# Performance work log

Hardware: AMD Instinct MI355X
Metric: run time of the kernel (lower is better)

The kernel has to match this reference:

```python
import jax, jax.numpy as jnp
from jax import lax
import numpy as np

DN = ('NHWC', 'HWIO', 'NHWC')  # NHWC activations, HWIO kernels (TF layout)
EPS = 1e-3


def setup_inputs() -> dict:
    key = jax.random.key(0)
    ks = jax.random.split(key, 6)
    B, H, W, C = 16, 64, 64, 256
    x = jax.random.normal(ks[0], (B, H, W, C), jnp.float32)
    # per-sample predicted kernels (scaled to keep activations well-conditioned)
    depthwise_kernels = jax.random.normal(ks[1], (B, 3, 3, C, C), jnp.float32) * 0.02
    pointwise_kernels = jax.random.normal(ks[2], (B, 1, 1, C, C), jnp.float32) * 0.06
    biases = jax.random.normal(ks[3], (B, C), jnp.float32) * 0.1
    # shared trailing Conv2D layer params
    conv_w = jax.random.normal(ks[4], (3, 3, C, C), jnp.float32) * 0.02
    conv_b = jnp.zeros((C,), jnp.float32)
    return dict(x=x, depthwise_kernels=depthwise_kernels,
                pointwise_kernels=pointwise_kernels, biases=biases,
                conv_w=conv_w, conv_b=conv_b)


def _instance_norm(x):
    # tf.nn.moments over spatial dims (population variance), eps=0.001
    mean = jnp.mean(x, axis=(1, 2), keepdims=True)
    var = jnp.var(x, axis=(1, 2), keepdims=True)
    return (x - mean) * lax.rsqrt(var + EPS)


def _reflect_pad_hw(x, p=1):
    pad = [(0, 0)] * (x.ndim - 3) + [(p, p), (p, p), (0, 0)]
    return jnp.pad(x, pad, mode='reflect')


def _per_sample_conv(xi, dk, pk, bi):
    # xi: [H,W,C]; dk: [3,3,C,Cm]; pk: [1,1,Cm,Co]; bi: [Co]
    xp = _reflect_pad_hw(xi)[None]  # [1,H+2,W+2,C]
    y = lax.conv_general_dilated(xp, dk, (1, 1), 'VALID', dimension_numbers=DN)
    y = lax.conv_general_dilated(y, pk, (1, 1), 'VALID', dimension_numbers=DN)
    return (y + bi)[0]


def reference(x, depthwise_kernels, pointwise_kernels, biases, conv_w, conv_b):
    x = _instance_norm(x)
    # per-sample kernels -> vmap over batch (replaces tf.map_fn)
    x = jax.vmap(_per_sample_conv)(x, depthwise_kernels, pointwise_kernels, biases)
    # shared Conv2D: reflect pad + VALID conv + bias
    xp = _reflect_pad_hw(x)
    y = lax.conv_general_dilated(xp, conv_w, (1, 1), 'VALID', dimension_numbers=DN)
    return y + conv_b
```

## Files before the change

kernel.cpp:

```cpp
#include <hip/hip_runtime.h>


typedef __bf16 bf16x8 __attribute__((ext_vector_type(8)));
typedef float f32x4 __attribute__((ext_vector_type(4)));

__device__ __forceinline__ float bf2f(unsigned short v) {
    return __uint_as_float(((unsigned int)v) << 16);
}
__device__ __forceinline__ unsigned short f2bf(float f) {
    unsigned int u = __float_as_uint(f);
    unsigned int r = (u + 0x7FFFu + ((u >> 16) & 1u)) >> 16;
    return (unsigned short)r;
}
__device__ __forceinline__ float ldg_elem(const void* p, size_t idx, bool isbf) {
    return isbf ? bf2f(((const unsigned short*)p)[idx]) : ((const float*)p)[idx];
}

__device__ __forceinline__ void gload16(const void* g, void* l) {
    __builtin_amdgcn_global_load_lds(
        (__attribute__((address_space(1))) void*)(unsigned long long)g,
        (__attribute__((address_space(3))) void*)(unsigned long long)l,
        16, 0, 0);
}

#define RAW_BARRIER() do { asm volatile("" ::: "memory"); \
                           __builtin_amdgcn_s_barrier();   \
                           asm volatile("" ::: "memory"); } while (0)

template <bool DO_DK>
__global__ void prep_kernel(const void* __restrict__ x, const void* __restrict__ pk,
                            const void* __restrict__ cw, const void* __restrict__ dk,
                            float* __restrict__ partS, float* __restrict__ partQ,
                            unsigned short* __restrict__ pkT, unsigned short* __restrict__ cwT,
                            unsigned short* __restrict__ dkT, int* __restrict__ flagp) {
    __shared__ int wild;
    __shared__ float red[4][64][9];
    __shared__ unsigned short tile[64][66];
    const int t = threadIdx.x;
    if (t == 0) wild = 0;
    __syncthreads();
    int cnt = 0;
    for (int i = 0; i < 16; ++i) {
        float a = fabsf(bf2f(((const unsigned short*)x)[t * 16 + i]));
        if (!(a < 64.f) || (a != 0.f && a < 1e-5f)) cnt++;
    }
    atomicAdd(&wild, cnt);
    __syncthreads();
    const bool isbf = (wild <= 512);
    const int id = blockIdx.x;
    if (id == 0 && t == 0) *flagp = isbf ? 1 : 0;

    if (id < 512) {
        const int b = id >> 5, ch = id & 31;
        const int l = t & 63;
        const int c4 = l * 4;
        const int sp0 = t >> 6;
        const size_t base = ((size_t)(b * 4096 + ch * 128 + sp0)) * 256 + c4;
        float s[4] = {0.f, 0.f, 0.f, 0.f}, q[4] = {0.f, 0.f, 0.f, 0.f};
        if (isbf) {
            for (int i = 0; i < 32; ++i) {
                ushort4 v = *(const ushort4*)((const unsigned short*)x + base + (size_t)i * 1024);
                float a[4] = {bf2f(v.x), bf2f(v.y), bf2f(v.z), bf2f(v.w)};
#pragma unroll
                for (int j = 0; j < 4; ++j) { s[j] += a[j]; q[j] += a[j] * a[j]; }
            }
        } else {
            for (int i = 0; i < 32; ++i) {
                float4 v = *(const float4*)((const float*)x + base + (size_t)i * 1024);
                float a[4] = {v.x, v.y, v.z, v.w};
#pragma unroll
                for (int j = 0; j < 4; ++j) { s[j] += a[j]; q[j] += a[j] * a[j]; }
            }
        }
#pragma unroll
        for (int j = 0; j < 4; ++j) { red[sp0][l][j] = s[j]; red[sp0][l][4 + j] = q[j]; }
        __syncthreads();
        if (t < 64) {
#pragma unroll
            for (int j = 0; j < 4; ++j) {
                float ss = red[0][t][j] + red[1][t][j] + red[2][t][j] + red[3][t][j];
                float qq = red[0][t][4 + j] + red[1][t][4 + j] + red[2][t][4 + j] + red[3][t][4 + j];
                int c = t * 4 + j;
                partS[(b * 32 + ch) * 256 + c] = ss;
                partQ[(b * 32 + ch) * 256 + c] = qq;
            }
        }
        return;
    }

    const void* src; unsigned short* dst; int s_per; long bstride; int coStride; int q;
    if (id < 768)      { q = id - 512; src = pk; dst = pkT; s_per = 1; bstride = 65536L;  coStride = 256;  }
    else if (id < 912) { q = id - 768; src = cw; dst = cwT; s_per = 9; bstride = 0L;      coStride = 2304; }
    else               { if (!DO_DK) return;
                         q = id - 912; src = dk; dst = dkT; s_per = 9; bstride = 589824L; coStride = 2304; }
    const int sl = q >> 4;
    const int ci0 = ((q >> 2) & 3) * 64, co0 = (q & 3) * 64;
    const int b = sl / s_per;
    const size_t dbase = (size_t)b * (size_t)bstride + (size_t)(sl % s_per) * 256;
    const int co4 = (t & 15) * 4;
    const int r0 = t >> 4;
#pragma unroll
    for (int i = 0; i < 4; ++i) {
        int r = r0 + i * 16;
        size_t sidx = (size_t)sl * 65536 + (size_t)(ci0 + r) * 256 + co0 + co4;
        if (isbf) {
            ushort4 v = *(const ushort4*)((const unsigned short*)src + sidx);
            tile[r][co4] = v.x; tile[r][co4 + 1] = v.y;
            tile[r][co4 + 2] = v.z; tile[r][co4 + 3] = v.w;
        } else {
            float4 v = *(const float4*)((const float*)src + sidx);
            tile[r][co4] = f2bf(v.x); tile[r][co4 + 1] = f2bf(v.y);
            tile[r][co4 + 2] = f2bf(v.z); tile[r][co4 + 3] = f2bf(v.w);
        }
    }
    __syncthreads();
    const int cip = (t & 31) * 2;
    const int cob = t >> 5;
#pragma unroll
    for (int i = 0; i < 8; ++i) {
        int co = cob + i * 8;
        *(unsigned int*)(dst + dbase + (size_t)(co0 + co) * coStride + ci0 + cip) =
            (unsigned int)tile[cip][co] | ((unsigned int)tile[cip + 1][co] << 16);
    }
}

__global__ void norm_finalize2(const float* __restrict__ partS, const float* __restrict__ partQ,
                               float* __restrict__ mean, float* __restrict__ rstd) {
    const int b = blockIdx.x, c = threadIdx.x;
    float s = 0.f, q = 0.f;
    for (int k = 0; k < 32; ++k) {
        s += partS[(b * 32 + k) * 256 + c];
        q += partQ[(b * 32 + k) * 256 + c];
    }
    float m = s * (1.f / 4096.f);
    float v = q * (1.f / 4096.f) - m * m;
    mean[b * 256 + c] = m;
    rstd[b * 256 + c] = rsqrtf(v + 1e-3f);
}

__global__ void norm_apply(const void* __restrict__ x, const int* __restrict__ flag,
                           const float* __restrict__ mean, const float* __restrict__ rstd,
                           unsigned short* __restrict__ xn) {
    const bool isbf = (*flag != 0);
    size_t e = ((size_t)blockIdx.x * 256 + threadIdx.x) * 8;
    int c0 = (int)(e & 255);
    int bc = (int)(e >> 20) * 256 + c0;
    float v[8];
    if (isbf) {
        uint4 raw = *(const uint4*)((const unsigned short*)x + e);
        unsigned int rr[4] = {raw.x, raw.y, raw.z, raw.w};
#pragma unroll
        for (int i = 0; i < 4; ++i) {
            v[2 * i]     = bf2f((unsigned short)(rr[i] & 0xFFFF));
            v[2 * i + 1] = bf2f((unsigned short)(rr[i] >> 16));
        }
    } else {
        float4 f0 = *(const float4*)((const float*)x + e);
        float4 f1 = *(const float4*)((const float*)x + e + 4);
        v[0] = f0.x; v[1] = f0.y; v[2] = f0.z; v[3] = f0.w;
        v[4] = f1.x; v[5] = f1.y; v[6] = f1.z; v[7] = f1.w;
    }
    unsigned int o[4];
#pragma unroll
    for (int i = 0; i < 4; ++i) {
        unsigned short lo = f2bf((v[2 * i]     - mean[bc + 2 * i])     * rstd[bc + 2 * i]);
        unsigned short hi = f2bf((v[2 * i + 1] - mean[bc + 2 * i + 1]) * rstd[bc + 2 * i + 1]);
        o[i] = (unsigned int)lo | ((unsigned int)hi << 16);
    }
    uint4 out; out.x = o[0]; out.y = o[1]; out.z = o[2]; out.w = o[3];
    *(uint4*)(xn + e) = out;
}

template <bool SCALE>
__global__ void transpose_wk(const void* __restrict__ src, const int* __restrict__ flag,
                             unsigned short* __restrict__ dst,
                             int s_per, long dstBStride, int coStride,
                             const float* __restrict__ rstd) {
    __shared__ unsigned short tile[64][66];
    const bool isbf = (*flag != 0);
    const int sl = blockIdx.x;
    const int b = sl / s_per;
    const size_t dbase = (size_t)b * (size_t)dstBStride + (size_t)(sl % s_per) * 256;
    const int ci0 = blockIdx.y * 64, co0 = blockIdx.z * 64;
    const int t = threadIdx.x;
    const int co4 = (t & 15) * 4;
    const int r0 = t >> 4;
#pragma unroll
    for (int i = 0; i < 4; ++i) {
        int r = r0 + i * 16;
        size_t sidx = (size_t)sl * 65536 + (size_t)(ci0 + r) * 256 + co0 + co4;
        if (isbf) {
            ushort4 v = *(const ushort4*)((const unsigned short*)src + sidx);
            tile[r][co4] = v.x; tile[r][co4 + 1] = v.y;
            tile[r][co4 + 2] = v.z; tile[r][co4 + 3] = v.w;
        } else {
            float4 v = *(const float4*)((const float*)src + sidx);
            tile[r][co4] = f2bf(v.x); tile[r][co4 + 1] = f2bf(v.y);
            tile[r][co4 + 2] = f2bf(v.z); tile[r][co4 + 3] = f2bf(v.w);
        }
    }
    __syncthreads();
    const int cip = (t & 31) * 2;
    const int cob = t >> 5;
    float s0 = 1.f, s1 = 1.f;
    if (SCALE) { s0 = rstd[b * 256 + ci0 + cip]; s1 = rstd[b * 256 + ci0 + cip + 1]; }
#pragma unroll
    for (int i = 0; i < 8; ++i) {
        int co = cob + i * 8;
        unsigned short lo = tile[cip][co], hi = tile[cip + 1][co];
        if (SCALE) { lo = f2bf(bf2f(lo) * s0); hi = f2bf(bf2f(hi) * s1); }
        *(unsigned int*)(dst + dbase + (size_t)(co0 + co) * coStride + ci0 + cip) =
            (unsigned int)lo | ((unsigned int)hi << 16);
    }
}

__global__ void corr_kernel(const unsigned short* __restrict__ dkT,
                            const float* __restrict__ mean,
                            float* __restrict__ negcorr) {
    const int b = blockIdx.x;
    const int lane = threadIdx.x & 63;
    const int co = blockIdx.y * 4 + (threadIdx.x >> 6);
    const unsigned short* wp = dkT + (size_t)(b * 256 + co) * 2304;
    const float* mb = mean + b * 256;
    const int ci0 = (lane & 31) * 8;
    float4 ma = *(const float4*)(mb + ci0);
    float4 mc = *(const float4*)(mb + ci0 + 4);
    float mm[8] = {ma.x, ma.y, ma.z, ma.w, mc.x, mc.y, mc.z, mc.w};
    float sum = 0.f;
#pragma unroll
    for (int c = 0; c < 5; ++c) {
        int k = c * 512 + lane * 8;
        if (k < 2304) {
            uint4 w = *(const uint4*)(wp + k);
            unsigned int wsv[4] = {w.x, w.y, w.z, w.w};
#pragma unroll
            for (int j = 0; j < 4; ++j) {
                sum += bf2f((unsigned short)(wsv[j] & 0xFFFF)) * mm[2 * j];
                sum += bf2f((unsigned short)(wsv[j] >> 16)) * mm[2 * j + 1];
            }
        }
    }
#pragma unroll
    for (int off = 32; off > 0; off >>= 1) sum += __shfl_down(sum, off);
    if (lane == 0) negcorr[b * 256 + co] = -sum;
}

template <bool PER_SAMPLE_W, int BIAS_MODE, bool OUT_F32>
__global__ __launch_bounds__(512, 2) void conv3x3_256(const unsigned short* __restrict__ src,
                                                      const int* __restrict__ flag,
                                                      const unsigned short* __restrict__ wT,
                                                      const void* __restrict__ bias,
                                                      void* __restrict__ dst) {
    constexpr int KTOT = 2304;
    extern __shared__ unsigned short smem[];

    const int t = threadIdx.x;
    const int lane = t & 63;
    const int wave = t >> 6;
    const int wr = wave >> 2;
    const int wc = wave & 3;
    const int bid = blockIdx.x + 16 * blockIdx.z;
    const int b  = (bid & 7) + ((bid >> 3) & 1) * 8;
    const int mt = bid >> 4;
    const int m0 = mt * 256;
    const int R0 = mt * 4;
    const unsigned short* srcB = src + (size_t)b * (4096 * 256);
    const unsigned short* wB = wT + (PER_SAMPLE_W ? (size_t)b * 256 * KTOT : (size_t)0);
    const bool in_bf = (BIAS_MODE >= 2) ? (*flag != 0) : true;

    const int wx = t >> 3;
    const int wg = ((t & 7) ^ (wx & 7)) << 3;
    int wrow[6];
#pragma unroll
    for (int u = 0; u < 6; ++u) {
        int r = R0 - 1 + u;
        wrow[u] = (r < 0) ? 1 : (r > 63 ? 62 : r);
    }
    const unsigned short* winsrc[6];
#pragma unroll
    for (int u = 0; u < 6; ++u)
        winsrc[u] = srcB + ((size_t)wrow[u] * 64 + wx) * 256 + wg;
    const unsigned short* bsrc = wB + (size_t)wx * KTOT + wg;

    f32x4 acc[8][4];
#pragma unroll
    for (int i = 0; i < 8; ++i)
#pragma unroll
        for (int j = 0; j < 4; ++j) acc[i][j] = (f32x4){0.f, 0.f, 0.f, 0.f};

    const int fr = lane & 15;
    const int quad = lane >> 4;
    const int fsw = fr & 7;
    const int ksb0 = (quad ^ fsw) << 3;
    const int ksb1 = ((quad + 4) ^ fsw) << 3;
    const int rm = wr * 128;
    const int cn = wc * 64;

#pragma unroll
    for (int u = 0; u < 6; ++u)
        gload16(winsrc[u], smem + u * 4096 + wave * 512);
#pragma unroll
    for (int u = 0; u < 4; ++u)
        gload16(bsrc + (size_t)u * 64 * KTOT, smem + 49152 + u * 4096 + wave * 512);

    bf16x8 af[4][2], bfr[4][2];

    for (int cg = 0; cg < 4; ++cg) {
        const unsigned short* winb = smem + (cg & 1) * 24576;
        for (int s = 0; s < 9; ++s) {
            const int j = cg * 9 + s;
            const int dh = s / 3 - 1;
            const int dw = s % 3 - 1;

            if (s == 6 || s == 7)      asm volatile("s_waitcnt vmcnt(2)" ::: "memory");
            else if (s == 8)           asm volatile("s_waitcnt vmcnt(1)" ::: "memory");
            else                       asm volatile("s_waitcnt vmcnt(0)" ::: "memory");
            RAW_BARRIER();

            if (j < 35) {
                const int s1 = (s == 8) ? 0 : s + 1;
                const int cg1 = (s == 8) ? cg + 1 : cg;
                const int koff1 = s1 * 256 + cg1 * 64;
                unsigned short* bdst = smem + 49152 + ((j + 1) & 1) * 16384 + wave * 512;
#pragma unroll
                for (int u = 0; u < 4; ++u)
                    gload16(bsrc + (size_t)u * 64 * KTOT + koff1, bdst + u * 4096);
            }
            if (cg < 3) {
                unsigned short* wdst = smem + ((cg + 1) & 1) * 24576 + wave * 512;
                const int cgo = (cg + 1) * 64;
                if (s == 5) {
                    gload16(winsrc[0] + cgo, wdst);
                    gload16(winsrc[1] + cgo, wdst + 4096);
                } else if (s == 6) {
                    gload16(winsrc[2] + cgo, wdst + 2 * 4096);
                    gload16(winsrc[3] + cgo, wdst + 3 * 4096);
                } else if (s == 7) {
                    gload16(winsrc[4] + cgo, wdst + 4 * 4096);
                } else if (s == 8) {
                    gload16(winsrc[5] + cgo, wdst + 5 * 4096);
                }
            }

            int aoo[4][2];
#pragma unroll
            for (int mi = 0; mi < 4; ++mi) {
                int ww = mi * 16 + fr + dw;
                ww = (ww < 0) ? 1 : (ww > 63 ? 62 : ww);
                const int x7 = ww & 7;
                aoo[mi][0] = ww * 64 + ((quad ^ x7) << 3);
                aoo[mi][1] = ww * 64 + (((quad + 4) ^ x7) << 3);
            }
            const unsigned short* A1 = winb + (wr * 2 + 1 + dh) * 4096;
            const unsigned short* A2 = A1 + 4096;
            const unsigned short* Bb = smem + 49152 + (j & 1) * 16384;

#pragma unroll
            for (int mi = 0; mi < 4; ++mi) {
                af[mi][0] = *(const bf16x8*)(A1 + aoo[mi][0]);
                af[mi][1] = *(const bf16x8*)(A1 + aoo[mi][1]);
            }
#pragma unroll
            for (int n = 0; n < 2; ++n) {
                const unsigned short* rp = Bb + (cn + n * 16 + fr) * 64;
                bfr[n][0] = *(const bf16x8*)(rp + ksb0);
                bfr[n][1] = *(const bf16x8*)(rp + ksb1);
            }
            __builtin_amdgcn_s_setprio(1);
#pragma unroll
            for (int mi = 0; mi < 4; ++mi)
#pragma unroll
                for (int n = 0; n < 2; ++n) {
                    acc[mi][n] = __builtin_amdgcn_mfma_f32_16x16x32_bf16(af[mi][0], bfr[n][0], acc[mi][n], 0, 0, 0);
                    acc[mi][n] = __builtin_amdgcn_mfma_f32_16x16x32_bf16(af[mi][1], bfr[n][1], acc[mi][n], 0, 0, 0);
                }
            __builtin_amdgcn_s_setprio(0);

#pragma unroll
            for (int n = 2; n < 4; ++n) {
                const unsigned short* rp = Bb + (cn + n * 16 + fr) * 64;
                bfr[n][0] = *(const bf16x8*)(rp + ksb0);
                bfr[n][1] = *(const bf16x8*)(rp + ksb1);
            }
            __builtin_amdgcn_s_setprio(1);
#pragma unroll
            for (int mi = 0; mi < 4; ++mi)
#pragma unroll
                for (int n = 2; n < 4; ++n) {
                    acc[mi][n] = __builtin_amdgcn_mfma_f32_16x16x32_bf16(af[mi][0], bfr[n][0], acc[mi][n], 0, 0, 0);
                    acc[mi][n] = __builtin_amdgcn_mfma_f32_16x16x32_bf16(af[mi][1], bfr[n][1], acc[mi][n], 0, 0, 0);
                }
            __builtin_amdgcn_s_setprio(0);

#pragma unroll
            for (int mi = 0; mi < 4; ++mi) {
                af[mi][0] = *(const bf16x8*)(A2 + aoo[mi][0]);
                af[mi][1] = *(const bf16x8*)(A2 + aoo[mi][1]);
            }
            __builtin_amdgcn_s_setprio(1);
#pragma unroll
            for (int mi = 0; mi < 4; ++mi)
#pragma unroll
                for (int n = 0; n < 4; ++n) {
                    acc[4 + mi][n] = __builtin_amdgcn_mfma_f32_16x16x32_bf16(af[mi][0], bfr[n][0], acc[4 + mi][n], 0, 0, 0);
                    acc[4 + mi][n] = __builtin_amdgcn_mfma_f32_16x16x32_bf16(af[mi][1], bfr[n][1], acc[4 + mi][n], 0, 0, 0);
                }
            __builtin_amdgcn_s_setprio(0);
        }
    }

    const int rbase = quad * 4;
    float bv[4];
#pragma unroll
    for (int n = 0; n < 4; ++n) {
        int nn = cn + n * 16 + fr;
        if (BIAS_MODE == 2)      bv[n] = ldg_elem(bias, b * 256 + nn, in_bf);
        else if (BIAS_MODE == 3) bv[n] = ldg_elem(bias, nn, in_bf);
        else                     bv[n] = 0.f;
    }
#pragma unroll
    for (int m = 0; m < 8; ++m) {
#pragma unroll
        for (int rr = 0; rr < 4; ++rr) {
            int mm = m0 + rm + m * 16 + rbase + rr;
            size_t rowoff = ((size_t)b * 4096 + mm) * 256;
#pragma unroll
            for (int n = 0; n < 4; ++n) {
                int nn = cn + n * 16 + fr;
                float val = acc[m][n][rr] + bv[n];
                if (OUT_F32) ((float*)dst)[rowoff + nn] = val;
                else         ((unsigned short*)dst)[rowoff + nn] = f2bf(val);
            }
        }
    }
}

template <int KSLICES, bool PER_SAMPLE_W, int BIAS_MODE, bool IS3X3, bool OUT_F32>
__global__ __launch_bounds__(512, 2) void gemm_conv_256(const unsigned short* __restrict__ src,
                                                        const int* __restrict__ flag,
                                                        const unsigned short* __restrict__ wT,
                                                        const void* __restrict__ bias,
                                                        void* __restrict__ dst) {
    constexpr int KTOT = KSLICES * 256;
    constexpr int NKT = KTOT / 64;
    static_assert(NKT >= 2, "pipeline needs >=2 K-tiles");
    extern __shared__ unsigned short smem[];

    const int t = threadIdx.x;
    const int lane = t & 63;
    const int wave = t >> 6;
    const int wr = wave >> 2;
    const int wc = wave & 3;
    const int bid = blockIdx.x + 16 * blockIdx.z;
    const int b  = (bid & 7) + ((bid >> 3) & 1) * 8;
    const int m0 = (bid >> 4) * 256;
    const unsigned short* srcB = src + (size_t)b * (4096 * 256);
    const unsigned short* wB = wT + (PER_SAMPLE_W ? (size_t)b * 256 * KTOT : (size_t)0);
    const bool in_bf = (BIAS_MODE >= 2) ? (*flag != 0) : true;

    const int trow = t >> 3;
    const int tswz = ((t & 7) ^ (trow & 7)) << 3;
    int hU[4], wU[4];
#pragma unroll
    for (int u = 0; u < 4; ++u) {
        int m = m0 + u * 64 + trow;
        hU[u] = m >> 6; wU[u] = m & 63;
    }
    const unsigned short* gBu[4];
#pragma unroll
    for (int u = 0; u < 4; ++u)
        gBu[u] = wB + (size_t)(u * 64 + trow) * KTOT + tswz;

    f32x4 acc[8][4];
#pragma unroll
    for (int i = 0; i < 8; ++i)
#pragma unroll
        for (int j = 0; j < 4; ++j) acc[i][j] = (f32x4){0.f, 0.f, 0.f, 0.f};

    const int fr = lane & 15;
    const int quad = lane >> 4;
    const int fsw = fr & 7;
    const int ks0 = ((quad) ^ fsw) << 3;
    const int ks1 = ((quad + 4) ^ fsw) << 3;
    const int rm = wr * 128;
    const int cn = wc * 64;

#pragma unroll
    for (int kt = 0; kt < 2; ++kt) {
        const int pdh = IS3X3 ? -1 : 0;
        const int pdw = IS3X3 ? -1 : 0;
        const int pchb = (kt & 3) << 6;
        unsigned short* ldsAW = smem + kt * 32768 + wave * 512;
#pragma unroll
        for (int u = 0; u < 4; ++u) {
            int hh = hU[u] + pdh; hh = (hh < 0) ? 1 : (hh > 63 ? 62 : hh);
            int ww = wU[u] + pdw; ww = (ww < 0) ? 1 : (ww > 63 ? 62 : ww);
            gload16(srcB + (size_t)((hh << 6) + ww) * 256 + pchb + tswz, ldsAW + u * 4096);
        }
#pragma unroll
        for (int u = 0; u < 4; ++u)
            gload16(gBu[u] + (size_t)kt * 64, ldsAW + 16384 + u * 4096);
    }
    asm volatile("s_waitcnt vmcnt(8)" ::: "memory");
    RAW_BARRIER();

    bf16x8 af[4][2], bfr[4][2];
    size_t aoff[4];
    int cur_s = -1;

    for (int i = 0; i < NKT; ++i) {
        const int buf = i & 1;
        const unsigned short* As_b = smem + buf * 32768;
        const unsigned short* Bs_b = As_b + 16384;
        unsigned short* ldsAW = smem + buf * 32768 + wave * 512;
        const int kt2 = i + 2;
        const bool st = (kt2 < NKT);

#pragma unroll
        for (int m = 0; m < 4; ++m) {
            const unsigned short* rp = As_b + (rm + m * 16 + fr) * 64;
            af[m][0] = *(const bf16x8*)(rp + ks0);
            af[m][1] = *(const bf16x8*)(rp + ks1);
        }
#pragma unroll
        for (int n = 0; n < 2; ++n) {
            const unsigned short* rp = Bs_b + (cn + n * 16 + fr) * 64;
            bfr[n][0] = *(const bf16x8*)(rp + ks0);
            bfr[n][1] = *(const bf16x8*)(rp + ks1);
        }
        __builtin_amdgcn_s_setprio(1);
#pragma unroll
        for (int m = 0; m < 4; ++m)
#pragma unroll
            for (int n = 0; n < 2; ++n) {
                acc[m][n] = __builtin_amdgcn_mfma_f32_16x16x32_bf16(af[m][0], bfr[n][0], acc[m][n], 0, 0, 0);
                acc[m][n] = __builtin_amdgcn_mfma_f32_16x16x32_bf16(af[m][1], bfr[n][1], acc[m][n], 0, 0, 0);
            }
        __builtin_amdgcn_s_setprio(0);

#pragma unroll
        for (int n = 2; n < 4; ++n) {
            const unsigned short* rp = Bs_b + (cn + n * 16 + fr) * 64;
            bfr[n][0] = *(const bf16x8*)(rp + ks0);
            bfr[n][1] = *(const bf16x8*)(rp + ks1);
        }
        __builtin_amdgcn_s_setprio(1);
#pragma unroll
        for (int m = 0; m < 4; ++m)
#pragma unroll
            for (int n = 2; n < 4; ++n) {
                acc[m][n] = __builtin_amdgcn_mfma_f32_16x16x32_bf16(af[m][0], bfr[n][0], acc[m][n], 0, 0, 0);
                acc[m][n] = __builtin_amdgcn_mfma_f32_16x16x32_bf16(af[m][1], bfr[n][1], acc[m][n], 0, 0, 0);
            }
        __builtin_amdgcn_s_setprio(0);

#pragma unroll
        for (int m = 0; m < 4; ++m) {
            const unsigned short* rp = As_b + (rm + 64 + m * 16 + fr) * 64;
            af[m][0] = *(const bf16x8*)(rp + ks0);
            af[m][1] = *(const bf16x8*)(rp + ks1);
        }
        __builtin_amdgcn_s_setprio(1);
#pragma unroll
        for (int m = 0; m < 4; ++m)
#pragma unroll
            for (int n = 0; n < 4; ++n) {
                acc[4 + m][n] = __builtin_amdgcn_mfma_f32_16x16x32_bf16(af[m][0], bfr[n][0], acc[4 + m][n], 0, 0, 0);
                acc[4 + m][n] = __builtin_amdgcn_mfma_f32_16x16x32_bf16(af[m][1], bfr[n][1], acc[4 + m][n], 0, 0, 0);
            }
        __builtin_amdgcn_s_setprio(0);

        RAW_BARRIER();
        if (st) {
            if (IS3X3) {
                const int s2 = kt2 >> 2;
                if (s2 != cur_s) {
                    cur_s = s2;
                    const int dh2 = s2 / 3 - 1, dw2 = s2 % 3 - 1;
#pragma unroll
                    for (int u = 0; u < 4; ++u) {
                        int hh = hU[u] + dh2; hh = (hh < 0) ? 1 : (hh > 63 ? 62 : hh);
                        int ww = wU[u] + dw2; ww = (ww < 0) ? 1 : (ww > 63 ? 62 : ww);
                        aoff[u] = (size_t)((hh << 6) + ww) * 256 + tswz;
                    }
                }
            } else if (cur_s < 0) {
                cur_s = 0;
#pragma unroll
                for (int u = 0; u < 4; ++u)
                    aoff[u] = (size_t)((hU[u] << 6) + wU[u]) * 256 + tswz;
            }
            const int chb2 = (kt2 & 3) << 6;
#pragma unroll
            for (int u = 0; u < 4; ++u)
                gload16(srcB + aoff[u] + chb2, ldsAW + u * 4096);
#pragma unroll
            for (int u = 0; u < 4; ++u)
                gload16(gBu[u] + (size_t)kt2 * 64, ldsAW + 16384 + u * 4096);
            asm volatile("s_waitcnt vmcnt(8)" ::: "memory");
        } else if (i + 1 < NKT) {
            asm volatile("s_waitcnt vmcnt(0)" ::: "memory");
        }
        RAW_BARRIER();
    }

    const int rbase = quad * 4;
    float bv[4];
#pragma unroll
    for (int n = 0; n < 4; ++n) {
        int nn = cn + n * 16 + fr;
        if (BIAS_MODE == 2)      bv[n] = ldg_elem(bias, b * 256 + nn, in_bf);
        else if (BIAS_MODE == 3) bv[n] = ldg_elem(bias, nn, in_bf);
        else                     bv[n] = 0.f;
    }
#pragma unroll
    for (int m = 0; m < 8; ++m) {
#pragma unroll
        for (int rr = 0; rr < 4; ++rr) {
            int mm = m0 + rm + m * 16 + rbase + rr;
            size_t rowoff = ((size_t)b * 4096 + mm) * 256;
#pragma unroll
            for (int n = 0; n < 4; ++n) {
                int nn = cn + n * 16 + fr;
                float val = acc[m][n][rr] + bv[n];
                if (OUT_F32) ((float*)dst)[rowoff + nn] = val;
                else         ((unsigned short*)dst)[rowoff + nn] = f2bf(val);
            }
        }
    }
}

template <int KSLICES, bool PER_SAMPLE_W, int BIAS_MODE, bool IS3X3, bool SRC_ADAPT, bool OUT_F32>
__global__ __launch_bounds__(256) void gemm_conv(const void* __restrict__ src,
                                                 const int* __restrict__ flag,
                                                 const unsigned short* __restrict__ wT,
                                                 const void* __restrict__ bias,
                                                 void* __restrict__ dst) {
    constexpr int KTOT = KSLICES * 256;
    __shared__ unsigned short As[128][40];
    __shared__ unsigned short Bs[128][40];

    const bool in_bf = (SRC_ADAPT || BIAS_MODE >= 2) ? (*flag != 0) : true;
    const int t = threadIdx.x;
    const int b = blockIdx.z;
    const int m0 = blockIdx.x * 128;
    const int n0 = blockIdx.y * 128;
    const size_t srcOfs = (size_t)b * (4096 * 256);
    const unsigned short* wB = wT + (PER_SAMPLE_W ? (size_t)b * 256 * KTOT : (size_t)0);

    f32x4 acc[4][4];
#pragma unroll
    for (int i = 0; i < 4; ++i)
#pragma unroll
        for (int j = 0; j < 4; ++j) acc[i][j] = (f32x4){0.f, 0.f, 0.f, 0.f};

    const int lane = t & 63;
    const int wave = t >> 6;
    const int rm = (wave >> 1) * 64;
    const int cn = (wave & 1) * 64;
    const int fr = lane & 15;
    const int kg = (lane >> 4) * 8;

    for (int kk = 0; kk < KTOT / 32; ++kk) {
        const int k0 = kk * 32;
        const int s = k0 >> 8;
        const int ci0 = k0 & 255;
        const int dh = IS3X3 ? (s / 3) - 1 : 0;
        const int dw = IS3X3 ? (s % 3) - 1 : 0;
        __syncthreads();
#pragma unroll
        for (int cc = 0; cc < 2; ++cc) {
            int ch = t + cc * 256;
            int r = ch >> 2;
            int ko = (ch & 3) << 3;
            int m = m0 + r;
            int h = m >> 6, w = m & 63;
            if (IS3X3) {
                h += dh; h = (h < 0) ? 1 : (h > 63 ? 62 : h);
                w += dw; w = (w < 0) ? 1 : (w > 63 ? 62 : w);
            }
            size_t eidx = srcOfs + (size_t)((h << 6) + w) * 256 + ci0 + ko;
            if (!SRC_ADAPT || in_bf) {
                uint4 v = *(const uint4*)((const unsigned short*)src + eidx);
                *(uint4*)&As[r][ko] = v;
            } else {
                const float* sf = (const float*)src + eidx;
                float4 f0 = *(const float4*)sf;
                float4 f1 = *(const float4*)(sf + 4);
                uint4 v;
                v.x = (unsigned int)f2bf(f0.x) | ((unsigned int)f2bf(f0.y) << 16);
                v.y = (unsigned int)f2bf(f0.z) | ((unsigned int)f2bf(f0.w) << 16);
                v.z = (unsigned int)f2bf(f1.x) | ((unsigned int)f2bf(f1.y) << 16);
                v.w = (unsigned int)f2bf(f1.z) | ((unsigned int)f2bf(f1.w) << 16);
                *(uint4*)&As[r][ko] = v;
            }
        }
#pragma unroll
        for (int cc = 0; cc < 2; ++cc) {
            int ch = t + cc * 256;
            int n = ch >> 2;
            int ko = (ch & 3) << 3;
            uint4 v = *(const uint4*)(wB + (size_t)(n0 + n) * KTOT + k0 + ko);
            *(uint4*)&Bs[n][ko] = v;
        }
        __syncthreads();

        bf16x8 af[4], bfr[4];
#pragma unroll
        for (int i = 0; i < 4; ++i) af[i] = *(const bf16x8*)&As[rm + i * 16 + fr][kg];
#pragma unroll
        for (int j = 0; j < 4; ++j) bfr[j] = *(const bf16x8*)&Bs[cn + j * 16 + fr][kg];
#pragma unroll
        for (int i = 0; i < 4; ++i)
#pragma unroll
            for (int j = 0; j < 4; ++j)
                acc[i][j] = __builtin_amdgcn_mfma_f32_16x16x32_bf16(af[i], bfr[j], acc[i][j], 0, 0, 0);
    }

    const int rbase = (lane >> 4) * 4;
    const int col = lane & 15;
    float bv[4];
#pragma unroll
    for (int j = 0; j < 4; ++j) {
        int n = n0 + cn + j * 16 + col;
        if (BIAS_MODE == 1)      bv[j] = ((const float*)bias)[b * 256 + n];
        else if (BIAS_MODE == 2) bv[j] = ldg_elem(bias, b * 256 + n, in_bf);
        else if (BIAS_MODE == 3) bv[j] = ldg_elem(bias, n, in_bf);
        else                     bv[j] = 0.f;
    }
#pragma unroll
    for (int i = 0; i < 4; ++i) {
#pragma unroll
        for (int rr = 0; rr < 4; ++rr) {
            int m = m0 + rm + i * 16 + rbase + rr;
            size_t rowoff = ((size_t)b * 4096 + m) * 256;
#pragma unroll
            for (int j = 0; j < 4; ++j) {
                int n = n0 + cn + j * 16 + col;
                float val = acc[i][j][rr] + bv[j];
                if (OUT_F32) ((float*)dst)[rowoff + n] = val;
                else         ((unsigned short*)dst)[rowoff + n] = f2bf(val);
            }
        }
    }
}

extern "C" void kernel_launch(void* const* d_in, const int* in_sizes, int n_in,
                              void* d_out, int out_size, void* d_ws, size_t ws_size,
                              hipStream_t stream) {
    const void* x    = d_in[0];
    const void* dk   = d_in[1];
    const void* pk   = d_in[2];
    const void* bias = d_in[3];
    const void* cw   = d_in[4];
    const void* cb   = d_in[5];

    const size_t NEED_SMALL = 36896768u;
    const size_t NEED_BIG   = 55771136u;
    if (ws_size < NEED_SMALL) return;
    const bool big = (ws_size >= NEED_BIG);

    char* ws = (char*)d_ws;
    int*   flagp   = (int*)ws;
    float* meanp   = (float*)(ws + 1024);
    float* rstdp   = (float*)(ws + 17408);
    float* negcorr = (float*)(ws + 33792);
    unsigned short* pkT = (unsigned short*)(ws + 65536);
    unsigned short* cwT = (unsigned short*)(ws + 2162688);
    unsigned short* dkT = (unsigned short*)(ws + 3342336);
    unsigned short* xn  = (unsigned short*)(ws + 22216704);
    float* partS = (float*)(ws + 22216704);
    float* partQ = (float*)(ws + 22216704 + 524288);
    unsigned short* y2  = big ? xn : dkT;
    unsigned short* y1  = (unsigned short*)d_out;

    hipFuncSetAttribute(reinterpret_cast<const void*>(conv3x3_256<true, 0, false>),
                        hipFuncAttributeMaxDynamicSharedMemorySize, 163840);
    hipFuncSetAttribute(reinterpret_cast<const void*>(conv3x3_256<false, 3, true>),
                        hipFuncAttributeMaxDynamicSharedMemorySize, 163840);
    hipFuncSetAttribute(reinterpret_cast<const void*>(gemm_conv_256<1, true, 2, false, false>),
                        hipFuncAttributeMaxDynamicSharedMemorySize, 131072);

    if (big) {
        prep_kernel<true><<<3216, 256, 0, stream>>>(x, pk, cw, dk, partS, partQ,
                                                    pkT, cwT, dkT, flagp);
        norm_finalize2<<<16, 256, 0, stream>>>(partS, partQ, meanp, rstdp);
        norm_apply<<<8192, 256, 0, stream>>>(x, flagp, meanp, rstdp, xn);
        conv3x3_256<true, 0, false><<<dim3(16, 1, 16), 512, 163840, stream>>>(xn, flagp, dkT, nullptr, y1);
    } else {
        prep_kernel<false><<<912, 256, 0, stream>>>(x, pk, cw, dk, partS, partQ,
                                                    pkT, cwT, dkT, flagp);
        norm_finalize2<<<16, 256, 0, stream>>>(partS, partQ, meanp, rstdp);
        transpose_wk<true><<<dim3(144, 4, 4), 256, 0, stream>>>(dk, flagp, dkT, 9, 589824L, 2304, rstdp);
        corr_kernel<<<dim3(16, 64), 256, 0, stream>>>(dkT, meanp, negcorr);
        gemm_conv<9, true, 1, true, true, false><<<dim3(32, 2, 16), 256, 0, stream>>>(x, flagp, dkT, negcorr, y1);
    }

    gemm_conv_256<1, true, 2, false, false><<<dim3(16, 1, 16), 512, 131072, stream>>>(y1, flagp, pkT, bias, y2);
    conv3x3_256<false, 3, true><<<dim3(16, 1, 16), 512, 163840, stream>>>(y2, flagp, cwT, cb, d_out);
}
```

Baseline: 342.2 us.

## Use 4-wave blocks with 128x128 warp tiles in conv3x3 kernel

Rebuilds the 3x3 conv kernel around 256-thread blocks: each of the 4 waves now computes a 128x128 output tile (8x8 MFMA accumulators) instead of 8 waves computing 128x64. This raises MFMA work per LDS fragment load and halves redundant A-fragment reads. Global-to-LDS loads are reissued with twice as many per-thread copies, and window prefetch is spread across steps 3-8. The cost is a much larger register footprint (256 accumulator floats per lane), fewer waves to hide latency, and launch bounds of 1 block per CU.

```diff
diff --git a/kernel.cpp b/kernel.cpp
--- a/kernel.cpp
+++ b/kernel.cpp
@@ -246,7 +246,7 @@
 }
 
 template <bool PER_SAMPLE_W, int BIAS_MODE, bool OUT_F32>
-__global__ __launch_bounds__(512, 2) void conv3x3_256(const unsigned short* __restrict__ src,
+__global__ __launch_bounds__(256, 1) void conv3x3_256(const unsigned short* __restrict__ src,
                                                       const int* __restrict__ flag,
                                                       const unsigned short* __restrict__ wT,
                                                       const void* __restrict__ bias,
@@ -257,8 +257,8 @@
     const int t = threadIdx.x;
     const int lane = t & 63;
     const int wave = t >> 6;
-    const int wr = wave >> 2;
-    const int wc = wave & 3;
+    const int wr = wave >> 1;
+    const int wc = wave & 1;
     const int bid = blockIdx.x + 16 * blockIdx.z;
     const int b  = (bid & 7) + ((bid >> 3) & 1) * 8;
     const int mt = bid >> 4;
@@ -282,28 +282,35 @@
         winsrc[u] = srcB + ((size_t)wrow[u] * 64 + wx) * 256 + wg;
     const unsigned short* bsrc = wB + (size_t)wx * KTOT + wg;
 
-    f32x4 acc[8][4];
+    auto issueWin = [&](int wbuf, int u, int cgo) {
+        unsigned short* wdst = smem + wbuf * 24576 + u * 4096 + wave * 512;
+        gload16(winsrc[u] + cgo, wdst);
+        gload16(winsrc[u] + cgo + 8192, wdst + 2048);
+    };
+    auto issueB = [&](int jn) {
+        const int sn = jn % 9, cgn = jn / 9;
+        const int koff = sn * 256 + cgn * 64;
+        unsigned short* bdst = smem + 49152 + (jn & 1) * 16384 + wave * 512;
+#pragma unroll
+        for (int u = 0; u < 8; ++u)
+            gload16(bsrc + (size_t)u * 32 * KTOT + koff, bdst + u * 2048);
+    };
+
+    f32x4 acc[8][8];
 #pragma unroll
     for (int i = 0; i < 8; ++i)
 #pragma unroll
-        for (int j = 0; j < 4; ++j) acc[i][j] = (f32x4){0.f, 0.f, 0.f, 0.f};
+        for (int j = 0; j < 8; ++j) acc[i][j] = (f32x4){0.f, 0.f, 0.f, 0.f};
 
     const int fr = lane & 15;
     const int quad = lane >> 4;
-    const int fsw = fr & 7;
-    const int ksb0 = (quad ^ fsw) << 3;
-    const int ksb1 = ((quad + 4) ^ fsw) << 3;
-    const int rm = wr * 128;
-    const int cn = wc * 64;
-
-#pragma unroll
-    for (int u = 0; u < 6; ++u)
-        gload16(winsrc[u], smem + u * 4096 + wave * 512);
-#pragma unroll
-    for (int u = 0; u < 4; ++u)
-        gload16(bsrc + (size_t)u * 64 * KTOT, smem + 49152 + u * 4096 + wave * 512);
-
-    bf16x8 af[4][2], bfr[4][2];
+    const int cn = wc * 128;
+
+#pragma unroll
+    for (int u = 0; u < 6; ++u) issueWin(0, u, 0);
+    issueB(0);
+
+    bf16x8 af[8], bfr[8];
 
     for (int cg = 0; cg < 4; ++cg) {
         const unsigned short* winb = smem + (cg & 1) * 24576;
@@ -312,122 +319,68 @@
             const int dh = s / 3 - 1;
             const int dw = s % 3 - 1;
 
-            if (s == 6 || s == 7)      asm volatile("s_waitcnt vmcnt(2)" ::: "memory");
-            else if (s == 8)           asm volatile("s_waitcnt vmcnt(1)" ::: "memory");
-            else                       asm volatile("s_waitcnt vmcnt(0)" ::: "memory");
+            const bool keep2 = (cg < 3) && (s >= 4) && (s <= 8);
+            if (keep2) asm volatile("s_waitcnt vmcnt(2)" ::: "memory");
+            else       asm volatile("s_waitcnt vmcnt(0)" ::: "memory");
             RAW_BARRIER();
 
-            if (j < 35) {
-                const int s1 = (s == 8) ? 0 : s + 1;
-                const int cg1 = (s == 8) ? cg + 1 : cg;
-                const int koff1 = s1 * 256 + cg1 * 64;
-                unsigned short* bdst = smem + 49152 + ((j + 1) & 1) * 16384 + wave * 512;
-#pragma unroll
-                for (int u = 0; u < 4; ++u)
-                    gload16(bsrc + (size_t)u * 64 * KTOT + koff1, bdst + u * 4096);
-            }
-            if (cg < 3) {
-                unsigned short* wdst = smem + ((cg + 1) & 1) * 24576 + wave * 512;
-                const int cgo = (cg + 1) * 64;
-                if (s == 5) {
-                    gload16(winsrc[0] + cgo, wdst);
-                    gload16(winsrc[1] + cgo, wdst + 4096);
-                } else if (s == 6) {
-                    gload16(winsrc[2] + cgo, wdst + 2 * 4096);
-                    gload16(winsrc[3] + cgo, wdst + 3 * 4096);
-                } else if (s == 7) {
-                    gload16(winsrc[4] + cgo, wdst + 4 * 4096);
-                } else if (s == 8) {
-                    gload16(winsrc[5] + cgo, wdst + 5 * 4096);
-                }
-            }
-
-            int aoo[4][2];
+            if (j < 35) issueB(j + 1);
+            if (cg < 3 && s >= 3) issueWin((cg + 1) & 1, s - 3, (cg + 1) * 64);
+
+            const unsigned short* Ar0 = winb + (wr * 2 + 1 + dh) * 4096;
+            const unsigned short* Ar1 = Ar0 + 4096;
+            const unsigned short* Bb = smem + 49152 + (j & 1) * 16384;
+            int aww[4];
 #pragma unroll
             for (int mi = 0; mi < 4; ++mi) {
                 int ww = mi * 16 + fr + dw;
-                ww = (ww < 0) ? 1 : (ww > 63 ? 62 : ww);
-                const int x7 = ww & 7;
-                aoo[mi][0] = ww * 64 + ((quad ^ x7) << 3);
-                aoo[mi][1] = ww * 64 + (((quad + 4) ^ x7) << 3);
-            }
-            const unsigned short* A1 = winb + (wr * 2 + 1 + dh) * 4096;
-            const unsigned short* A2 = A1 + 4096;
-            const unsigned short* Bb = smem + 49152 + (j & 1) * 16384;
-
-#pragma unroll
-            for (int mi = 0; mi < 4; ++mi) {
-                af[mi][0] = *(const bf16x8*)(A1 + aoo[mi][0]);
-                af[mi][1] = *(const bf16x8*)(A1 + aoo[mi][1]);
-            }
-#pragma unroll
-            for (int n = 0; n < 2; ++n) {
-                const unsigned short* rp = Bb + (cn + n * 16 + fr) * 64;
-                bfr[n][0] = *(const bf16x8*)(rp + ksb0);
-                bfr[n][1] = *(const bf16x8*)(rp + ksb1);
-            }
-            __builtin_amdgcn_s_setprio(1);
-#pragma unroll
-            for (int mi = 0; mi < 4; ++mi)
-#pragma unroll
-                for (int n = 0; n < 2; ++n) {
-                    acc[mi][n] = __builtin_amdgcn_mfma_f32_16x16x32_bf16(af[mi][0], bfr[n][0], acc[mi][n], 0, 0, 0);
-                    acc[mi][n] = __builtin_amdgcn_mfma_f32_16x16x32_bf16(af[mi][1], bfr[n][1], acc[mi][n], 0, 0, 0);
+                aww[mi] = (ww < 0) ? 1 : (ww > 63 ? 62 : ww);
+            }
+
+#pragma unroll
+            for (int h = 0; h < 2; ++h) {
+                const int kq = (h << 2) + quad;
+#pragma unroll
+                for (int mi = 0; mi < 4; ++mi) {
+                    const int ao = aww[mi] * 64 + ((kq ^ (aww[mi] & 7)) << 3);
+                    af[mi]     = *(const bf16x8*)(Ar0 + ao);
+                    af[mi + 4] = *(const bf16x8*)(Ar1 + ao);
                 }
-            __builtin_amdgcn_s_setprio(0);
-
-#pragma unroll
-            for (int n = 2; n < 4; ++n) {
-                const unsigned short* rp = Bb + (cn + n * 16 + fr) * 64;
-                bfr[n][0] = *(const bf16x8*)(rp + ksb0);
-                bfr[n][1] = *(const bf16x8*)(rp + ksb1);
-            }
-            __builtin_amdgcn_s_setprio(1);
-#pragma unroll
-            for (int mi = 0; mi < 4; ++mi)
-#pragma unroll
-                for (int n = 2; n < 4; ++n) {
-                    acc[mi][n] = __builtin_amdgcn_mfma_f32_16x16x32_bf16(af[mi][0], bfr[n][0], acc[mi][n], 0, 0, 0);
-                    acc[mi][n] = __builtin_amdgcn_mfma_f32_16x16x32_bf16(af[mi][1], bfr[n][1], acc[mi][n], 0, 0, 0);
+#pragma unroll
+                for (int n = 0; n < 8; ++n) {
+                    const int co = cn + n * 16 + fr;
+                    bfr[n] = *(const bf16x8*)(Bb + co * 64 + ((kq ^ (co & 7)) << 3));
                 }
-            __builtin_amdgcn_s_setprio(0);
-
-#pragma unroll
-            for (int mi = 0; mi < 4; ++mi) {
-                af[mi][0] = *(const bf16x8*)(A2 + aoo[mi][0]);
-                af[mi][1] = *(const bf16x8*)(A2 + aoo[mi][1]);
-            }
-            __builtin_amdgcn_s_setprio(1);
-#pragma unroll
-            for (int mi = 0; mi < 4; ++mi)
-#pragma unroll
-                for (int n = 0; n < 4; ++n) {
-                    acc[4 + mi][n] = __builtin_amdgcn_mfma_f32_16x16x32_bf16(af[mi][0], bfr[n][0], acc[4 + mi][n], 0, 0, 0);
-                    acc[4 + mi][n] = __builtin_amdgcn_mfma_f32_16x16x32_bf16(af[mi][1], bfr[n][1], acc[4 + mi][n], 0, 0, 0);
-                }
-            __builtin_amdgcn_s_setprio(0);
+                __builtin_amdgcn_s_setprio(1);
+#pragma unroll
+                for (int mi = 0; mi < 8; ++mi)
+#pragma unroll
+                    for (int n = 0; n < 8; ++n)
+                        acc[mi][n] = __builtin_amdgcn_mfma_f32_16x16x32_bf16(af[mi], bfr[n], acc[mi][n], 0, 0, 0);
+                __builtin_amdgcn_s_setprio(0);
+            }
         }
     }
 
     const int rbase = quad * 4;
-    float bv[4];
-#pragma unroll
-    for (int n = 0; n < 4; ++n) {
+    float bv[8];
+#pragma unroll
+    for (int n = 0; n < 8; ++n) {
         int nn = cn + n * 16 + fr;
         if (BIAS_MODE == 2)      bv[n] = ldg_elem(bias, b * 256 + nn, in_bf);
         else if (BIAS_MODE == 3) bv[n] = ldg_elem(bias, nn, in_bf);
         else                     bv[n] = 0.f;
     }
 #pragma unroll
-    for (int m = 0; m < 8; ++m) {
+    for (int mi = 0; mi < 8; ++mi) {
 #pragma unroll
         for (int rr = 0; rr < 4; ++rr) {
-            int mm = m0 + rm + m * 16 + rbase + rr;
+            int mm = m0 + wr * 128 + (mi >> 2) * 64 + (mi & 3) * 16 + rbase + rr;
             size_t rowoff = ((size_t)b * 4096 + mm) * 256;
 #pragma unroll
-            for (int n = 0; n < 4; ++n) {
+            for (int n = 0; n < 8; ++n) {
                 int nn = cn + n * 16 + fr;
-                float val = acc[m][n][rr] + bv[n];
+                float val = acc[mi][n][rr] + bv[n];
                 if (OUT_F32) ((float*)dst)[rowoff + nn] = val;
                 else         ((unsigned short*)dst)[rowoff + nn] = f2bf(val);
             }
@@ -786,7 +739,7 @@
                                                     pkT, cwT, dkT, flagp);
         norm_finalize2<<<16, 256, 0, stream>>>(partS, partQ, meanp, rstdp);
         norm_apply<<<8192, 256, 0, stream>>>(x, flagp, meanp, rstdp, xn);
-        conv3x3_256<true, 0, false><<<dim3(16, 1, 16), 512, 163840, stream>>>(xn, flagp, dkT, nullptr, y1);
+        conv3x3_256<true, 0, false><<<dim3(16, 1, 16), 256, 163840, stream>>>(xn, flagp, dkT, nullptr, y1);
     } else {
         prep_kernel<false><<<912, 256, 0, stream>>>(x, pk, cw, dk, partS, partQ,
                                                     pkT, cwT, dkT, flagp);
@@ -797,5 +750,5 @@
     }
 
     gemm_conv_256<1, true, 2, false, false><<<dim3(16, 1, 16), 512, 131072, stream>>>(y1, flagp, pkT, bias, y2);
-    conv3x3_256<false, 3, true><<<dim3(16, 1, 16), 512, 163840, stream>>>(y2, flagp, cwT, cb, d_out);
-}
+    conv3x3_256<false, 3, true><<<dim3(16, 1, 16), 256, 163840, stream>>>(y2, flagp, cwT, cb, d_out);
+}
```

Result: slower. 350.8 us (+2.5%).
